# Performance work log

Measured on AMD Instinct MI355X. Metric: run time of the kernel, lower is better.

The kernel has to match this reference:

```python
import jax, jax.numpy as jnp
import numpy as np
import math

B, W, BINS, BANDS = 2, 2048, 1024, 8  # cropsize == W
HEAD = BINS // BANDS


def setup_inputs() -> dict:
    key = jax.random.key(0)
    ks = jax.random.split(key, 10)
    s = 1.0 / math.sqrt(BINS)
    return {
        "x": jax.random.normal(ks[0], (B, W, BINS), jnp.float32),
        "Wq": jax.random.normal(ks[1], (BINS, BINS), jnp.float32) * s,
        "bq": jax.random.normal(ks[2], (BINS,), jnp.float32) * s,
        "Wk": jax.random.normal(ks[3], (BINS, BINS), jnp.float32) * s,
        "bk": jax.random.normal(ks[4], (BINS,), jnp.float32) * s,
        "Wv": jax.random.normal(ks[5], (BINS, BINS), jnp.float32) * s,
        "bv": jax.random.normal(ks[6], (BINS,), jnp.float32) * s,
        "Wo": jax.random.normal(ks[7], (BINS, BINS), jnp.float32) * s,
        "bo": jax.random.normal(ks[8], (BINS,), jnp.float32) * s,
        "er": jax.random.normal(ks[9], (HEAD, W), jnp.float32) * s,  # [bins//num_bands, cropsize]
    }


def reference(x, Wq, bq, Wk, bk, Wv, bv, Wo, bo, er):
    b, w, h = x.shape
    n = BANDS
    # projections -> [b, n, w, head]
    q = (x @ Wq.T + bq).reshape(b, w, n, -1).transpose(0, 2, 1, 3)
    k = (x @ Wk.T + bk).reshape(b, w, n, -1).transpose(0, 2, 1, 3)
    v = (x @ Wv.T + bv).reshape(b, w, n, -1).transpose(0, 2, 1, 3)
    # relative position bias via skew trick: [b, n, w, cropsize]
    qer = jnp.einsum('bnwd,dc->bnwc', q, er)
    p = jnp.pad(qer, ((0, 0), (0, 0), (0, 0), (1, 0)))  # pad left of last dim
    p = jnp.swapaxes(p, 2, 3)[:, :, 1:, :]              # [b, n, w, w]
    a = (jnp.einsum('bnqd,bnkd->bnqk', q, k) + p) / math.sqrt(h)
    attn = jax.nn.softmax(a, axis=-1)
    ctx = jnp.einsum('bnqk,bnkd->bnqd', attn, v).transpose(0, 2, 1, 3).reshape(b, w, h)
    o = ctx @ Wo.T + bo
    return (o, a)
```

## Files before the change

kernel.cpp:

```cpp
#include <hip/hip_runtime.h>

typedef __attribute__((ext_vector_type(8))) __bf16 bf16x8;
typedef __attribute__((ext_vector_type(4))) float f32x4;

__device__ __forceinline__ unsigned short f2bf(float f) {
  __bf16 h = (__bf16)f;
  return __builtin_bit_cast(unsigned short, h);
}

__device__ __forceinline__ f32x4 mfma_bf16(bf16x8 a, bf16x8 b, f32x4 c) {
  return __builtin_amdgcn_mfma_f32_16x16x32_bf16(a, b, c, 0, 0, 0);
}

__device__ __forceinline__ void gload_lds16(const void* g, void* l) {
  __builtin_amdgcn_global_load_lds((const __attribute__((address_space(1))) void*)g,
                                   (__attribute__((address_space(3))) void*)l, 16, 0, 0);
}


__global__ void cvt_f32_bf16(const float* __restrict__ in, unsigned short* __restrict__ out, int n4) {
  int i = blockIdx.x * blockDim.x + threadIdx.x;
  if (i < n4) {
    float4 v = reinterpret_cast<const float4*>(in)[i];
    ushort4 o;
    o.x = f2bf(v.x); o.y = f2bf(v.y); o.z = f2bf(v.z); o.w = f2bf(v.w);
    reinterpret_cast<ushort4*>(out)[i] = o;
  }
}

__global__ void cvt4_f32_bf16(const float* __restrict__ a, const float* __restrict__ b,
                              const float* __restrict__ c, const float* __restrict__ d,
                              unsigned short* __restrict__ oa, unsigned short* __restrict__ ob,
                              unsigned short* __restrict__ oc, unsigned short* __restrict__ od) {
  int i = blockIdx.x * blockDim.x + threadIdx.x;
  int which = i >> 18, j = i & 262143;
  const float* src = (which == 0) ? a : (which == 1) ? b : (which == 2) ? c : d;
  unsigned short* dst = (which == 0) ? oa : (which == 1) ? ob : (which == 2) ? oc : od;
  float4 v = reinterpret_cast<const float4*>(src)[j];
  ushort4 o;
  o.x = f2bf(v.x); o.y = f2bf(v.y); o.z = f2bf(v.z); o.w = f2bf(v.w);
  reinterpret_cast<ushort4*>(dst)[j] = o;
}

__global__ void er_transpose(const float* __restrict__ er, unsigned short* __restrict__ ert) {
  __shared__ float t[32][33];
  int w0 = blockIdx.x * 32, d0 = blockIdx.y * 32;
  int tx = threadIdx.x, ty = threadIdx.y;
#pragma unroll
  for (int i = 0; i < 4; ++i)
    t[ty + i * 8][tx] = er[(size_t)(d0 + ty + i * 8) * 2048 + w0 + tx];
  __syncthreads();
#pragma unroll
  for (int i = 0; i < 4; ++i)
    ert[(size_t)(w0 + ty + i * 8) * 128 + d0 + tx] = f2bf(t[tx][ty + i * 8]);
}


__global__ __launch_bounds__(512, 1) void gemm_qkv3(
    const unsigned short* __restrict__ xb,
    const unsigned short* __restrict__ Wqb, const unsigned short* __restrict__ Wkb,
    const unsigned short* __restrict__ Wvb,
    const float* __restrict__ bq, const float* __restrict__ bk, const float* __restrict__ bvv,
    unsigned short* __restrict__ Qb, unsigned short* __restrict__ Kb,
    unsigned short* __restrict__ Vtb)
{
  __shared__ __align__(16) char lds[131072];

  const int tid = threadIdx.x;
  const int lane = tid & 63, wid = tid >> 6;
  const int lr = lane & 15, lq = lane >> 4;
  const int wr = wid >> 1, wc = wid & 1;
  const int i0 = blockIdx.x * 128, j0 = blockIdx.y * 128;

  f32x4 aQ[2][4] = {}, aK[2][4] = {}, aV[2][4] = {};

  int ldso[2];
  const char *asrc[2], *qsrc[2], *ksrc[2], *vsrc[2];
#pragma unroll
  for (int p = 0; p < 2; ++p) {
    int L = p * 8192 + tid * 16;
    int row = L >> 7, colb = L & 127;
    int sc = colb ^ ((row & 7) << 4);
    ldso[p] = L;
    asrc[p] = (const char*)xb  + (size_t)(i0 + row) * 2048 + sc;
    qsrc[p] = (const char*)Wqb + (size_t)(j0 + row) * 2048 + sc;
    ksrc[p] = (const char*)Wkb + (size_t)(j0 + row) * 2048 + sc;
    vsrc[p] = (const char*)Wvb + (size_t)(j0 + row) * 2048 + sc;
  }

#pragma unroll
  for (int p = 0; p < 2; ++p) gload_lds16(asrc[p], lds + ldso[p]);
#pragma unroll
  for (int p = 0; p < 2; ++p) gload_lds16(qsrc[p], lds + 16384 + ldso[p]);
#pragma unroll
  for (int p = 0; p < 2; ++p) gload_lds16(ksrc[p], lds + 32768 + ldso[p]);
#pragma unroll
  for (int p = 0; p < 2; ++p) gload_lds16(vsrc[p], lds + 49152 + ldso[p]);

  const int swz = (lr & 7) << 4;

  for (int kt = 0; kt < 16; ++kt) {
    char* cb = lds + (kt & 1) * 65536;
    char* nb = lds + ((kt + 1) & 1) * 65536;

    asm volatile("s_waitcnt vmcnt(0)" ::: "memory");
    __builtin_amdgcn_sched_barrier(0);
    __builtin_amdgcn_s_barrier();
    __builtin_amdgcn_sched_barrier(0);

    if (kt < 15) {
      const int k0b = (kt + 1) * 128;
#pragma unroll
      for (int p = 0; p < 2; ++p) gload_lds16(asrc[p] + k0b, nb + ldso[p]);
#pragma unroll
      for (int p = 0; p < 2; ++p) gload_lds16(qsrc[p] + k0b, nb + 16384 + ldso[p]);
#pragma unroll
      for (int p = 0; p < 2; ++p) gload_lds16(ksrc[p] + k0b, nb + 32768 + ldso[p]);
#pragma unroll
      for (int p = 0; p < 2; ++p) gload_lds16(vsrc[p] + k0b, nb + 49152 + ldso[p]);
    }
    __builtin_amdgcn_sched_barrier(0);

#pragma unroll
    for (int kk = 0; kk < 2; ++kk) {
      const int coff = (kk * 64 + lq * 16) ^ swz;
      bf16x8 af[2];
#pragma unroll
      for (int m = 0; m < 2; ++m)
        af[m] = *(const bf16x8*)(cb + (wr * 32 + m * 16 + lr) * 128 + coff);
      bf16x8 bq_[4], bk_[4], bv_[4];
#pragma unroll
      for (int n = 0; n < 4; ++n) {
        const int rb = (wc * 64 + n * 16 + lr) * 128 + coff;
        bq_[n] = *(const bf16x8*)(cb + 16384 + rb);
        bk_[n] = *(const bf16x8*)(cb + 32768 + rb);
        bv_[n] = *(const bf16x8*)(cb + 49152 + rb);
      }
      __builtin_amdgcn_s_setprio(1);
#pragma unroll
      for (int m = 0; m < 2; ++m)
#pragma unroll
        for (int n = 0; n < 4; ++n) {
          aQ[m][n] = mfma_bf16(af[m], bq_[n], aQ[m][n]);
          aK[m][n] = mfma_bf16(af[m], bk_[n], aK[m][n]);
          aV[m][n] = mfma_bf16(af[m], bv_[n], aV[m][n]);
        }
      __builtin_amdgcn_s_setprio(0);
    }
  }

  float vbq[4], vbk[4], vbv[4];
#pragma unroll
  for (int n = 0; n < 4; ++n) {
    int gj = j0 + wc * 64 + n * 16 + lr;
    vbq[n] = bq[gj]; vbk[n] = bk[gj]; vbv[n] = bvv[gj];
  }

#pragma unroll
  for (int m = 0; m < 2; ++m)
#pragma unroll
    for (int n = 0; n < 4; ++n)
#pragma unroll
      for (int r = 0; r < 4; ++r) {
        int gi = i0 + wr * 32 + m * 16 + lq * 4 + r;
        int gj = j0 + wc * 64 + n * 16 + lr;
        Qb[(size_t)gi * 1024 + gj] = f2bf(aQ[m][n][r] + vbq[n]);
        Kb[(size_t)gi * 1024 + gj] = f2bf(aK[m][n][r] + vbk[n]);
      }

  __syncthreads();
  unsigned short* lds16 = (unsigned short*)lds;
#pragma unroll
  for (int m = 0; m < 2; ++m)
#pragma unroll
    for (int n = 0; n < 4; ++n)
#pragma unroll
      for (int r = 0; r < 4; ++r) {
        int il = wr * 32 + m * 16 + lq * 4 + r;
        int jl = wc * 64 + n * 16 + lr;
        lds16[jl * 132 + il] = f2bf(aV[m][n][r] + vbv[n]);
      }
  __syncthreads();
  {
    const int b = i0 >> 11, w0 = i0 & 2047, bd = j0 >> 7;
    for (int idx = tid; idx < 16384; idx += 512) {
      int dl = idx >> 7, wl = idx & 127;
      Vtb[(size_t)((b * 8 + bd) * 128 + dl) * 2048 + w0 + wl] = lds16[dl * 132 + wl];
    }
  }
}


__global__ __launch_bounds__(256, 2) void gemm_bt(
    const unsigned short* __restrict__ A,
    const unsigned short* __restrict__ Bt,
    const float* __restrict__ bias,
    float* __restrict__ C)
{
  __shared__ __align__(16) char base[32768];

  const int tid = threadIdx.x;
  const int lane = tid & 63, wid = tid >> 6;
  const int lr = lane & 15, lq = lane >> 4;
  const int wr = wid >> 1, wc = wid & 1;
  const int i0 = blockIdx.x * 128, j0 = blockIdx.y * 128;

  f32x4 acc[4][4] = {};

  const char* Abase = (const char*)A + (size_t)(i0 + (tid >> 2)) * 2048 + ((tid & 3) << 4);
  const char* Bbase = (const char*)Bt + (size_t)(j0 + (tid >> 2)) * 2048 + ((tid & 3) << 4);

  gload_lds16(Abase,             base + tid * 16);
  gload_lds16(Abase + 64 * 2048, base + 4096 + tid * 16);
  gload_lds16(Bbase,             base + 8192 + tid * 16);
  gload_lds16(Bbase + 64 * 2048, base + 12288 + tid * 16);

  for (int kt = 0; kt < 32; ++kt) {
    char* cbuf = base + (kt & 1) * 16384;
    char* nbuf = base + ((kt + 1) & 1) * 16384;

    asm volatile("s_waitcnt vmcnt(0)" ::: "memory");
    __builtin_amdgcn_sched_barrier(0);
    __builtin_amdgcn_s_barrier();
    __builtin_amdgcn_sched_barrier(0);

    if (kt < 31) {
      const int k0b = (kt + 1) * 64;
      gload_lds16(Abase + k0b,             nbuf + tid * 16);
      gload_lds16(Abase + k0b + 64 * 2048, nbuf + 4096 + tid * 16);
      gload_lds16(Bbase + k0b,             nbuf + 8192 + tid * 16);
      gload_lds16(Bbase + k0b + 64 * 2048, nbuf + 12288 + tid * 16);
    }
    __builtin_amdgcn_sched_barrier(0);

    bf16x8 af[4], bfr[4];
#pragma unroll
    for (int m = 0; m < 4; ++m)
      af[m] = *(const bf16x8*)(cbuf + (wr * 64 + m * 16 + lr) * 64 + lq * 16);
#pragma unroll
    for (int n = 0; n < 4; ++n)
      bfr[n] = *(const bf16x8*)(cbuf + 8192 + (wc * 64 + n * 16 + lr) * 64 + lq * 16);
    __builtin_amdgcn_s_setprio(1);
#pragma unroll
    for (int m = 0; m < 4; ++m)
#pragma unroll
      for (int n = 0; n < 4; ++n)
        acc[m][n] = mfma_bf16(af[m], bfr[n], acc[m][n]);
    __builtin_amdgcn_s_setprio(0);
  }

  float bv[4];
#pragma unroll
  for (int n = 0; n < 4; ++n) bv[n] = bias[j0 + wc * 64 + n * 16 + lr];
#pragma unroll
  for (int m = 0; m < 4; ++m)
#pragma unroll
    for (int n = 0; n < 4; ++n)
#pragma unroll
      for (int r = 0; r < 4; ++r) {
        int gi = i0 + wr * 64 + m * 16 + lq * 4 + r;
        int gj = j0 + wc * 64 + n * 16 + lr;
        C[(size_t)gi * 1024 + gj] = acc[m][n][r] + bv[n];
      }
}


__global__ __launch_bounds__(512) void attn_fused(
    const unsigned short* __restrict__ Qb,
    const unsigned short* __restrict__ Kb,
    const unsigned short* __restrict__ Vt,
    const unsigned short* __restrict__ ErT,
    float* __restrict__ a_out,
    unsigned short* __restrict__ ctx)
{
  __shared__ __align__(16) char Klb[32768];
  __shared__ __align__(16) char Qlb[32768];
  __shared__ __align__(16) char Vlb[32768];
  __shared__ __align__(16) char Plb[32768];

  const int bb = blockIdx.x;
  const int bd = bb & 7, b = bb >> 3;
  const int qi0 = blockIdx.y * 128;
  const int tid = threadIdx.x, wid = tid >> 6, lane = tid & 63;
  const int lr = lane & 15, lq = lane >> 4;

  bf16x8 qf[4], ef[4];
  {
    const unsigned short* Qrow = Qb + (size_t)(b * 2048 + qi0 + wid * 16 + lr) * 1024 + bd * 128;
    const unsigned short* Erow = ErT + (size_t)(qi0 + wid * 16 + lr) * 128;
#pragma unroll
    for (int kk = 0; kk < 4; ++kk) {
      qf[kk] = *(const bf16x8*)(Qrow + kk * 32 + lq * 8);
      ef[kk] = *(const bf16x8*)(Erow + kk * 32 + lq * 8);
    }
  }

  int ldso[4];
  const char *ksrc[4], *qsrc[4], *vsrc[4];
#pragma unroll
  for (int p = 0; p < 4; ++p) {
    int L = p * 8192 + tid * 16;
    int row = L >> 8, cs = L & 255;
    int sc = cs ^ ((row & 7) << 4);
    ldso[p] = L;
    ksrc[p] = (const char*)Kb + ((size_t)(b * 2048 + row) * 1024 + bd * 128) * 2 + sc;
    qsrc[p] = (const char*)Qb + ((size_t)(b * 2048 + row) * 1024 + bd * 128) * 2 + sc;
    vsrc[p] = (const char*)Vt + ((size_t)(bb * 128 + row) * 2048) * 2 + sc;
  }

#pragma unroll
  for (int p = 0; p < 4; ++p) gload_lds16(ksrc[p], Klb + ldso[p]);
#pragma unroll
  for (int p = 0; p < 4; ++p) gload_lds16(qsrc[p], Qlb + ldso[p]);
#pragma unroll
  for (int p = 0; p < 4; ++p) gload_lds16(vsrc[p], Vlb + ldso[p]);
  asm volatile("s_waitcnt vmcnt(0)" ::: "memory");
  __builtin_amdgcn_sched_barrier(0);

  f32x4 oacc[8] = {};
  float M[4], L[4];
#pragma unroll
  for (int r = 0; r < 4; ++r) { M[r] = -1e30f; L[r] = 0.f; }

  float* abase = a_out + (size_t)bb * 2048 * 2048;

  for (int kt = 0; kt < 16; ++kt) {
    const int kj0 = kt * 128;
    const size_t nkq = (size_t)((kt + 1) & 15) * 262144;
    const size_t nv = (size_t)((kt + 1) & 15) * 256;

    asm volatile("s_waitcnt vmcnt(36)" ::: "memory");
    __builtin_amdgcn_sched_barrier(0);
    __builtin_amdgcn_s_barrier();
    __builtin_amdgcn_sched_barrier(0);

    f32x4 sacc[8] = {};
    __builtin_amdgcn_s_setprio(1);
#pragma unroll
    for (int kk = 0; kk < 4; ++kk) {
#pragma unroll
      for (int nf = 0; nf < 8; ++nf) {
        const int row = nf * 16 + lr;
        bf16x8 kf = *(const bf16x8*)(Klb + row * 256 + ((kk * 64 + lq * 16) ^ ((row & 7) << 4)));
        sacc[nf] = mfma_bf16(qf[kk], kf, sacc[nf]);
      }
#pragma unroll
      for (int nf = 0; nf < 8; ++nf) {
        const int row = nf * 16 + lr;
        bf16x8 qkf = *(const bf16x8*)(Qlb + row * 256 + ((kk * 64 + lq * 16) ^ ((row & 7) << 4)));
        sacc[nf] = mfma_bf16(ef[kk], qkf, sacc[nf]);
      }
    }
    __builtin_amdgcn_s_setprio(0);

    __builtin_amdgcn_sched_barrier(0);
    __builtin_amdgcn_s_barrier();
    __builtin_amdgcn_sched_barrier(0);

#pragma unroll
    for (int p = 0; p < 4; ++p) gload_lds16(ksrc[p] + nkq, Klb + ldso[p]);
#pragma unroll
    for (int p = 0; p < 4; ++p) gload_lds16(qsrc[p] + nkq, Qlb + ldso[p]);
    __builtin_amdgcn_sched_barrier(0);

#pragma unroll
    for (int nf = 0; nf < 8; ++nf)
#pragma unroll
      for (int r = 0; r < 4; ++r) sacc[nf][r] *= 0.03125f;
    {
      const int qrow_base = qi0 + wid * 16 + lq * 4;
#pragma unroll
      for (int nf = 0; nf < 8; ++nf)
#pragma unroll
        for (int r = 0; r < 4; ++r)
          abase[(size_t)(qrow_base + r) * 2048 + kj0 + nf * 16 + lr] = sacc[nf][r];
    }
    __builtin_amdgcn_sched_barrier(0);

    float rmax[4];
#pragma unroll
    for (int r = 0; r < 4; ++r) {
      float m0 = sacc[0][r];
#pragma unroll
      for (int nf = 1; nf < 8; ++nf) m0 = fmaxf(m0, sacc[nf][r]);
      m0 = fmaxf(m0, __shfl_xor(m0, 1));
      m0 = fmaxf(m0, __shfl_xor(m0, 2));
      m0 = fmaxf(m0, __shfl_xor(m0, 4));
      m0 = fmaxf(m0, __shfl_xor(m0, 8));
      rmax[r] = m0;
    }
    bool small = (rmax[0] - M[0] <= 8.f) & (rmax[1] - M[1] <= 8.f) &
                 (rmax[2] - M[2] <= 8.f) & (rmax[3] - M[3] <= 8.f);
    unsigned long long vote = __ballot(small);
    if (vote != ~0ull) {
      float scl[4];
#pragma unroll
      for (int r = 0; r < 4; ++r) {
        float Mn = fmaxf(M[r], rmax[r]);
        scl[r] = __expf(M[r] - Mn);
        M[r] = Mn;
        L[r] *= scl[r];
      }
#pragma unroll
      for (int dn = 0; dn < 8; ++dn)
#pragma unroll
        for (int r = 0; r < 4; ++r) oacc[dn][r] *= scl[r];
    }
    float rsum[4] = {0.f, 0.f, 0.f, 0.f};
#pragma unroll
    for (int nf = 0; nf < 8; ++nf)
#pragma unroll
      for (int r = 0; r < 4; ++r) {
        float pv = __expf(sacc[nf][r] - M[r]);
        sacc[nf][r] = pv;
        rsum[r] += pv;
      }
    {
      const int prow0 = wid * 16 + lq * 4;
#pragma unroll
      for (int nf = 0; nf < 8; ++nf)
#pragma unroll
        for (int r = 0; r < 4; ++r) {
          const int row = prow0 + r;
          *(unsigned short*)(Plb + row * 256 + (((nf * 16 + lr) * 2) ^ ((row & 7) << 4))) =
              f2bf(sacc[nf][r]);
        }
    }
#pragma unroll
    for (int r = 0; r < 4; ++r) {
      rsum[r] += __shfl_xor(rsum[r], 1);
      rsum[r] += __shfl_xor(rsum[r], 2);
      rsum[r] += __shfl_xor(rsum[r], 4);
      rsum[r] += __shfl_xor(rsum[r], 8);
      L[r] += rsum[r];
    }

    asm volatile("s_waitcnt vmcnt(40)" ::: "memory");
    __builtin_amdgcn_sched_barrier(0);

    __builtin_amdgcn_s_setprio(1);
#pragma unroll
    for (int kk = 0; kk < 4; ++kk) {
      const int prow = wid * 16 + lr;
      bf16x8 pf = *(const bf16x8*)(Plb + prow * 256 + ((kk * 64 + lq * 16) ^ ((prow & 7) << 4)));
#pragma unroll
      for (int dn = 0; dn < 8; ++dn) {
        const int vrow = dn * 16 + lr;
        bf16x8 vf = *(const bf16x8*)(Vlb + vrow * 256 + ((kk * 64 + lq * 16) ^ ((vrow & 7) << 4)));
        oacc[dn] = mfma_bf16(pf, vf, oacc[dn]);
      }
    }
    __builtin_amdgcn_s_setprio(0);

    __builtin_amdgcn_sched_barrier(0);
    __builtin_amdgcn_s_barrier();
    __builtin_amdgcn_sched_barrier(0);
#pragma unroll
    for (int p = 0; p < 4; ++p) gload_lds16(vsrc[p] + nv, Vlb + ldso[p]);
    __builtin_amdgcn_sched_barrier(0);
  }

  {
    const int qrow_base = b * 2048 + qi0 + wid * 16 + lq * 4;
#pragma unroll
    for (int dn = 0; dn < 8; ++dn)
#pragma unroll
      for (int r = 0; r < 4; ++r) {
        float v = oacc[dn][r] / L[r];
        ctx[(size_t)(qrow_base + r) * 1024 + bd * 128 + dn * 16 + lr] = f2bf(v);
      }
  }
}


extern "C" void kernel_launch(void* const* d_in, const int* in_sizes, int n_in,
                              void* d_out, int out_size, void* d_ws, size_t ws_size,
                              hipStream_t stream) {
  const float* x  = (const float*)d_in[0];
  const float* Wq = (const float*)d_in[1];
  const float* bq = (const float*)d_in[2];
  const float* Wk = (const float*)d_in[3];
  const float* bk = (const float*)d_in[4];
  const float* Wv = (const float*)d_in[5];
  const float* bv = (const float*)d_in[6];
  const float* Wo = (const float*)d_in[7];
  const float* bo = (const float*)d_in[8];
  const float* er = (const float*)d_in[9];

  char* ws = (char*)d_ws;
  unsigned short* xb  = (unsigned short*)(ws + 0);
  unsigned short* Wqb = (unsigned short*)(ws + 8388608);
  unsigned short* Wkb = (unsigned short*)(ws + 10485760);
  unsigned short* Wvb = (unsigned short*)(ws + 12582912);
  unsigned short* Wob = (unsigned short*)(ws + 14680064);
  unsigned short* Qb  = (unsigned short*)(ws + 16777216);
  unsigned short* Kb  = (unsigned short*)(ws + 25165824);
  unsigned short* Vtb = (unsigned short*)(ws + 33554432);
  unsigned short* ctx = (unsigned short*)(ws + 41943040);
  unsigned short* ert = (unsigned short*)(ws + 50331648);

  float* a_out = (float*)d_out + 4194304;

  cvt_f32_bf16<<<dim3(4096), dim3(256), 0, stream>>>(x, xb, 1048576);
  cvt4_f32_bf16<<<dim3(4096), dim3(256), 0, stream>>>(Wq, Wk, Wv, Wo, Wqb, Wkb, Wvb, Wob);
  er_transpose<<<dim3(64, 4), dim3(32, 8), 0, stream>>>(er, ert);

  gemm_qkv3<<<dim3(32, 8), dim3(512), 0, stream>>>(xb, Wqb, Wkb, Wvb, bq, bk, bv,
                                                   Qb, Kb, Vtb);

  attn_fused<<<dim3(16, 16), dim3(512), 0, stream>>>(Qb, Kb, Vtb, ert, a_out, ctx);

  gemm_bt<<<dim3(32, 8), dim3(256), 0, stream>>>(ctx, Wob, bo, (float*)d_out);
}
```

Baseline: 177.5 us.

## Merge prep kernels into one launch and retile output GEMM with swizzled LDS

Combines the x conversion, weight conversion and er transpose into a single prep launch to cut launch overhead. Rewrites the output projection GEMM to use 8 waves per block, a K step of 128, and an XOR-swizzled LDS layout to reduce bank conflicts and barrier count. This doubles LDS use per block, which may limit occupancy.

```diff
diff --git a/kernel.cpp b/kernel.cpp
--- a/kernel.cpp
+++ b/kernel.cpp
@@ -18,41 +18,44 @@
 }
 
 
-__global__ void cvt_f32_bf16(const float* __restrict__ in, unsigned short* __restrict__ out, int n4) {
-  int i = blockIdx.x * blockDim.x + threadIdx.x;
-  if (i < n4) {
-    float4 v = reinterpret_cast<const float4*>(in)[i];
+__global__ void prep_all(const float* __restrict__ x,
+                         const float* __restrict__ Wq, const float* __restrict__ Wk,
+                         const float* __restrict__ Wv, const float* __restrict__ Wo,
+                         const float* __restrict__ er,
+                         unsigned short* __restrict__ xb,
+                         unsigned short* __restrict__ Wqb, unsigned short* __restrict__ Wkb,
+                         unsigned short* __restrict__ Wvb, unsigned short* __restrict__ Wob,
+                         unsigned short* __restrict__ ert)
+{
+  const int bid = blockIdx.x, tid = threadIdx.x;
+  if (bid < 4096) {
+    int i = bid * 256 + tid;
+    float4 v = reinterpret_cast<const float4*>(x)[i];
     ushort4 o;
     o.x = f2bf(v.x); o.y = f2bf(v.y); o.z = f2bf(v.z); o.w = f2bf(v.w);
-    reinterpret_cast<ushort4*>(out)[i] = o;
-  }
-}
-
-__global__ void cvt4_f32_bf16(const float* __restrict__ a, const float* __restrict__ b,
-                              const float* __restrict__ c, const float* __restrict__ d,
-                              unsigned short* __restrict__ oa, unsigned short* __restrict__ ob,
-                              unsigned short* __restrict__ oc, unsigned short* __restrict__ od) {
-  int i = blockIdx.x * blockDim.x + threadIdx.x;
-  int which = i >> 18, j = i & 262143;
-  const float* src = (which == 0) ? a : (which == 1) ? b : (which == 2) ? c : d;
-  unsigned short* dst = (which == 0) ? oa : (which == 1) ? ob : (which == 2) ? oc : od;
-  float4 v = reinterpret_cast<const float4*>(src)[j];
-  ushort4 o;
-  o.x = f2bf(v.x); o.y = f2bf(v.y); o.z = f2bf(v.z); o.w = f2bf(v.w);
-  reinterpret_cast<ushort4*>(dst)[j] = o;
-}
-
-__global__ void er_transpose(const float* __restrict__ er, unsigned short* __restrict__ ert) {
-  __shared__ float t[32][33];
-  int w0 = blockIdx.x * 32, d0 = blockIdx.y * 32;
-  int tx = threadIdx.x, ty = threadIdx.y;
-#pragma unroll
-  for (int i = 0; i < 4; ++i)
-    t[ty + i * 8][tx] = er[(size_t)(d0 + ty + i * 8) * 2048 + w0 + tx];
-  __syncthreads();
-#pragma unroll
-  for (int i = 0; i < 4; ++i)
-    ert[(size_t)(w0 + ty + i * 8) * 128 + d0 + tx] = f2bf(t[tx][ty + i * 8]);
+    reinterpret_cast<ushort4*>(xb)[i] = o;
+  } else if (bid < 8192) {
+    int i = (bid - 4096) * 256 + tid;
+    int which = i >> 18, j = i & 262143;
+    const float* src = (which == 0) ? Wq : (which == 1) ? Wk : (which == 2) ? Wv : Wo;
+    unsigned short* dst = (which == 0) ? Wqb : (which == 1) ? Wkb : (which == 2) ? Wvb : Wob;
+    float4 v = reinterpret_cast<const float4*>(src)[j];
+    ushort4 o;
+    o.x = f2bf(v.x); o.y = f2bf(v.y); o.z = f2bf(v.z); o.w = f2bf(v.w);
+    reinterpret_cast<ushort4*>(dst)[j] = o;
+  } else {
+    __shared__ float t[32][33];
+    int blk = bid - 8192;
+    int w0 = (blk & 63) * 32, d0 = (blk >> 6) * 32;
+    int tx = tid & 31, ty = tid >> 5;
+#pragma unroll
+    for (int i = 0; i < 4; ++i)
+      t[ty + i * 8][tx] = er[(size_t)(d0 + ty + i * 8) * 2048 + w0 + tx];
+    __syncthreads();
+#pragma unroll
+    for (int i = 0; i < 4; ++i)
+      ert[(size_t)(w0 + ty + i * 8) * 128 + d0 + tx] = f2bf(t[tx][ty + i * 8]);
+  }
 }
 
 
@@ -191,13 +194,13 @@
 }
 
 
-__global__ __launch_bounds__(256, 2) void gemm_bt(
+__global__ __launch_bounds__(512, 4) void gemm_bt(
     const unsigned short* __restrict__ A,
     const unsigned short* __restrict__ Bt,
     const float* __restrict__ bias,
     float* __restrict__ C)
 {
-  __shared__ __align__(16) char base[32768];
+  __shared__ __align__(16) char lds[65536];
 
   const int tid = threadIdx.x;
   const int lane = tid & 63, wid = tid >> 6;
@@ -205,60 +208,76 @@
   const int wr = wid >> 1, wc = wid & 1;
   const int i0 = blockIdx.x * 128, j0 = blockIdx.y * 128;
 
-  f32x4 acc[4][4] = {};
-
-  const char* Abase = (const char*)A + (size_t)(i0 + (tid >> 2)) * 2048 + ((tid & 3) << 4);
-  const char* Bbase = (const char*)Bt + (size_t)(j0 + (tid >> 2)) * 2048 + ((tid & 3) << 4);
-
-  gload_lds16(Abase,             base + tid * 16);
-  gload_lds16(Abase + 64 * 2048, base + 4096 + tid * 16);
-  gload_lds16(Bbase,             base + 8192 + tid * 16);
-  gload_lds16(Bbase + 64 * 2048, base + 12288 + tid * 16);
-
-  for (int kt = 0; kt < 32; ++kt) {
-    char* cbuf = base + (kt & 1) * 16384;
-    char* nbuf = base + ((kt + 1) & 1) * 16384;
+  f32x4 acc[2][4] = {};
+
+  int ldso[2];
+  const char *asrc[2], *bsrc[2];
+#pragma unroll
+  for (int p = 0; p < 2; ++p) {
+    int L = p * 8192 + tid * 16;
+    int row = L >> 7, colb = L & 127;
+    int sc = colb ^ ((row & 7) << 4);
+    ldso[p] = L;
+    asrc[p] = (const char*)A  + (size_t)(i0 + row) * 2048 + sc;
+    bsrc[p] = (const char*)Bt + (size_t)(j0 + row) * 2048 + sc;
+  }
+
+#pragma unroll
+  for (int p = 0; p < 2; ++p) gload_lds16(asrc[p], lds + ldso[p]);
+#pragma unroll
+  for (int p = 0; p < 2; ++p) gload_lds16(bsrc[p], lds + 16384 + ldso[p]);
+
+  const int swz = (lr & 7) << 4;
+
+  for (int kt = 0; kt < 16; ++kt) {
+    char* cb = lds + (kt & 1) * 32768;
+    char* nb = lds + ((kt + 1) & 1) * 32768;
 
     asm volatile("s_waitcnt vmcnt(0)" ::: "memory");
     __builtin_amdgcn_sched_barrier(0);
     __builtin_amdgcn_s_barrier();
     __builtin_amdgcn_sched_barrier(0);
 
-    if (kt < 31) {
-      const int k0b = (kt + 1) * 64;
-      gload_lds16(Abase + k0b,             nbuf + tid * 16);
-      gload_lds16(Abase + k0b + 64 * 2048, nbuf + 4096 + tid * 16);
-      gload_lds16(Bbase + k0b,             nbuf + 8192 + tid * 16);
-      gload_lds16(Bbase + k0b + 64 * 2048, nbuf + 12288 + tid * 16);
-    }
-    __builtin_amdgcn_sched_barrier(0);
-
-    bf16x8 af[4], bfr[4];
-#pragma unroll
-    for (int m = 0; m < 4; ++m)
-      af[m] = *(const bf16x8*)(cbuf + (wr * 64 + m * 16 + lr) * 64 + lq * 16);
+    if (kt < 15) {
+      const int k0b = (kt + 1) * 128;
+#pragma unroll
+      for (int p = 0; p < 2; ++p) gload_lds16(asrc[p] + k0b, nb + ldso[p]);
+#pragma unroll
+      for (int p = 0; p < 2; ++p) gload_lds16(bsrc[p] + k0b, nb + 16384 + ldso[p]);
+    }
+    __builtin_amdgcn_sched_barrier(0);
+
+#pragma unroll
+    for (int kk = 0; kk < 2; ++kk) {
+      const int coff = (kk * 64 + lq * 16) ^ swz;
+      bf16x8 af[2];
+#pragma unroll
+      for (int m = 0; m < 2; ++m)
+        af[m] = *(const bf16x8*)(cb + (wr * 32 + m * 16 + lr) * 128 + coff);
+      bf16x8 bf_[4];
+#pragma unroll
+      for (int n = 0; n < 4; ++n)
+        bf_[n] = *(const bf16x8*)(cb + 16384 + (wc * 64 + n * 16 + lr) * 128 + coff);
+      __builtin_amdgcn_s_setprio(1);
+#pragma unroll
+      for (int m = 0; m < 2; ++m)
+#pragma unroll
+        for (int n = 0; n < 4; ++n)
+          acc[m][n] = mfma_bf16(af[m], bf_[n], acc[m][n]);
+      __builtin_amdgcn_s_setprio(0);
+    }
+  }
+
+  float bv[4];
+#pragma unroll
+  for (int n = 0; n < 4; ++n) bv[n] = bias[j0 + wc * 64 + n * 16 + lr];
+#pragma unroll
+  for (int m = 0; m < 2; ++m)
 #pragma unroll
     for (int n = 0; n < 4; ++n)
-      bfr[n] = *(const bf16x8*)(cbuf + 8192 + (wc * 64 + n * 16 + lr) * 64 + lq * 16);
-    __builtin_amdgcn_s_setprio(1);
-#pragma unroll
-    for (int m = 0; m < 4; ++m)
-#pragma unroll
-      for (int n = 0; n < 4; ++n)
-        acc[m][n] = mfma_bf16(af[m], bfr[n], acc[m][n]);
-    __builtin_amdgcn_s_setprio(0);
-  }
-
-  float bv[4];
-#pragma unroll
-  for (int n = 0; n < 4; ++n) bv[n] = bias[j0 + wc * 64 + n * 16 + lr];
-#pragma unroll
-  for (int m = 0; m < 4; ++m)
-#pragma unroll
-    for (int n = 0; n < 4; ++n)
 #pragma unroll
       for (int r = 0; r < 4; ++r) {
-        int gi = i0 + wr * 64 + m * 16 + lq * 4 + r;
+        int gi = i0 + wr * 32 + m * 16 + lq * 4 + r;
         int gj = j0 + wc * 64 + n * 16 + lr;
         C[(size_t)gi * 1024 + gj] = acc[m][n][r] + bv[n];
       }
@@ -501,14 +520,13 @@
 
   float* a_out = (float*)d_out + 4194304;
 
-  cvt_f32_bf16<<<dim3(4096), dim3(256), 0, stream>>>(x, xb, 1048576);
-  cvt4_f32_bf16<<<dim3(4096), dim3(256), 0, stream>>>(Wq, Wk, Wv, Wo, Wqb, Wkb, Wvb, Wob);
-  er_transpose<<<dim3(64, 4), dim3(32, 8), 0, stream>>>(er, ert);
+  prep_all<<<dim3(8448), dim3(256), 0, stream>>>(x, Wq, Wk, Wv, Wo, er,
+                                                 xb, Wqb, Wkb, Wvb, Wob, ert);
 
   gemm_qkv3<<<dim3(32, 8), dim3(512), 0, stream>>>(xb, Wqb, Wkb, Wvb, bq, bk, bv,
                                                    Qb, Kb, Vtb);
 
   attn_fused<<<dim3(16, 16), dim3(512), 0, stream>>>(Qb, Kb, Vtb, ert, a_out, ctx);
 
-  gemm_bt<<<dim3(32, 8), dim3(256), 0, stream>>>(ctx, Wob, bo, (float*)d_out);
-}
+  gemm_bt<<<dim3(32, 8), dim3(512), 0, stream>>>(ctx, Wob, bo, (float*)d_out);
+}
```

Result: faster. 171.1 us (-3.6%).
